# Optimization experiments

Hardware: AMD Instinct MI355X
Metric: run time of the kernel (lower is better)

Reference implementation:

```python
import jax, jax.numpy as jnp
import numpy as np

DIM = 2048
N_HEAD = 16
HEAD_DIM = DIM // N_HEAD


def setup_inputs() -> dict:
    key = jax.random.key(0)
    ks = jax.random.split(key, 7)
    B, N = 2, 2048
    s = 1.0 / np.sqrt(DIM)
    return {
        "x": jax.random.normal(ks[0], (B, N, DIM), dtype=jnp.float32),
        "Wq": jax.random.normal(ks[1], (DIM, DIM), dtype=jnp.float32) * s,
        "bq": jnp.zeros((DIM,), dtype=jnp.float32),
        "Wkv": jax.random.normal(ks[2], (DIM, 2 * HEAD_DIM), dtype=jnp.float32) * s,
        "bkv": jnp.zeros((2 * HEAD_DIM,), dtype=jnp.float32),
        "Wo": jax.random.normal(ks[3], (DIM, DIM), dtype=jnp.float32) * s,
        "bo": jnp.zeros((DIM,), dtype=jnp.float32),
    }


def reference(x, Wq, bq, Wkv, bkv, Wo, bo):
    B, N, D = x.shape
    # Q projection -> (B, H, N, hd)
    q = (x @ Wq + bq).reshape(B, N, N_HEAD, HEAD_DIM).transpose(0, 2, 1, 3)
    # shared single-head K/V (kv = x, self-attention path)
    kvp = x @ Wkv + bkv  # (B, M, 2*hd)
    k, v = kvp[..., :HEAD_DIM], kvp[..., HEAD_DIM:]  # (B, M, hd) each
    scale = 1.0 / np.sqrt(HEAD_DIM).astype(np.float32)
    # broadcast shared K over heads without materializing expanded K/V
    scores = jnp.einsum("bhnd,bmd->bhnm", q, k) * scale  # (B, H, N, M)
    attn = jax.nn.softmax(scores, axis=-1)
    out = jnp.einsum("bhnm,bmd->bhnd", attn, v)  # (B, H, N, hd)
    out = out.transpose(0, 2, 1, 3).reshape(B, N, D)
    return out @ Wo + bo
```

## Files before the change

kernel.cpp:

```cpp
#include <hip/hip_runtime.h>
#include <math.h>

using bf16x8 = __attribute__((ext_vector_type(8))) short;
using f32x4  = __attribute__((ext_vector_type(4))) float;
using f32x16 = __attribute__((ext_vector_type(16))) float;
using u16x4  = __attribute__((ext_vector_type(4))) unsigned short;
using u32x4  = __attribute__((ext_vector_type(4))) unsigned int;

#define DIMSZ 2048
#define NSEQ  2048
#define BATCH 2
#define NHEAD 16
#define HD    128

__device__ __forceinline__ unsigned short f2bf(float x) {
    unsigned int u = __builtin_bit_cast(unsigned int, x);
    unsigned int r = (u + 0x7FFFu + ((u >> 16) & 1u)) >> 16;
    return (unsigned short)r;
}

__device__ __forceinline__ unsigned int cvtpk_bf16(float lo, float hi) {
    unsigned int r;
    asm("v_cvt_pk_bf16_f32 %0, %1, %2" : "=v"(r) : "v"(lo), "v"(hi));
    return r;
}

__device__ __forceinline__ void gload_lds16(const unsigned short* g, unsigned short* l) {
    __builtin_amdgcn_global_load_lds(
        (const __attribute__((address_space(1))) unsigned int*)g,
        (__attribute__((address_space(3))) unsigned int*)l, 16, 0, 0);
}

#define NCAST 8192
__global__ void k_prep(const float* __restrict__ x, unsigned short* __restrict__ xb,
                       const float* __restrict__ Wq, const float* __restrict__ Wkv,
                       const float* __restrict__ Wo, unsigned short* __restrict__ wqkvt,
                       unsigned short* __restrict__ wot, float sc) {
    __shared__ float t[32][33];
    const int tid = threadIdx.x;
    if ((int)blockIdx.x < NCAST) {
        int i = blockIdx.x * 256 + tid;
        f32x4 v = *(const f32x4*)(x + (size_t)i * 4);
        u16x4 o;
#pragma unroll
        for (int j = 0; j < 4; j++) o[j] = f2bf(v[j]);
        *(u16x4*)(xb + (size_t)i * 4) = o;
        return;
    }
    const int tb = blockIdx.x - NCAST;
    const int ct = tb % 136;
    const int k0 = (tb / 136) * 32;
    const float* src;
    unsigned short* dst;
    float scale;
    int N, n0;
    if (ct < 64)      { src = Wq;  dst = wqkvt;                       scale = sc;   N = 2048; n0 = ct * 32; }
    else if (ct < 72) { src = Wkv; dst = wqkvt + (size_t)2048 * 2048; scale = 1.0f; N = 256;  n0 = (ct - 64) * 32; }
    else              { src = Wo;  dst = wot;                         scale = 1.0f; N = 2048; n0 = (ct - 72) * 32; }
    const int tx = tid & 31, ty = tid >> 5;
#pragma unroll
    for (int i = 0; i < 32; i += 8) t[ty + i][tx] = src[(size_t)(k0 + ty + i) * N + n0 + tx];
    __syncthreads();
#pragma unroll
    for (int i = 0; i < 32; i += 8)
        dst[(size_t)(n0 + ty + i) * 2048 + k0 + tx] = f2bf(t[tx][ty + i] * scale);
}

__device__ __forceinline__ void xcd_tile(int nbx, int& bx, int& by) {
    int wg = ((int)blockIdx.x & 7) * ((int)gridDim.x >> 3) + ((int)blockIdx.x >> 3);
    bx = wg % nbx;
    by = wg / nbx;
}

__global__ __launch_bounds__(256, 2)
void k_gemm_qkv(const unsigned short* __restrict__ A, const unsigned short* __restrict__ Bt,
                const float* __restrict__ bq, float bscale, const float* __restrict__ bkv,
                unsigned short* __restrict__ qout, unsigned short* __restrict__ kvout,
                unsigned short* __restrict__ vtout, int M, int K, int nbx) {
    __shared__ unsigned short As[2][128 * 32];
    __shared__ unsigned short Bs[2][128 * 32];
    const int tid = threadIdx.x;
    const int wid = tid >> 6;
    const int lane = tid & 63;
    const int g = lane >> 4, cc = lane & 15;
    const int wr = wid >> 1, wc = wid & 1;
    int bx, by;
    xcd_tile(nbx, bx, by);
    const size_t m0 = (size_t)by * 128;
    const size_t n0 = (size_t)bx * 128;

    f32x4 acc[4][4] = {};

    const int srow = wid * 32 + (lane >> 2);
    const int sch = lane & 3;
    const unsigned short* gA = A + (m0 + srow) * (size_t)K + sch * 8;
    const unsigned short* gB = Bt + (n0 + srow) * (size_t)K + sch * 8;
    const int lo = wid * 32 * 32;

    auto STAGE = [&](int buf, int k0) {
        gload_lds16(gA + k0, &As[buf][lo]);
        gload_lds16(gA + 16 * (size_t)K + k0, &As[buf][lo + 16 * 32]);
        gload_lds16(gB + k0, &Bs[buf][lo]);
        gload_lds16(gB + 16 * (size_t)K + k0, &Bs[buf][lo + 16 * 32]);
    };

    STAGE(0, 0);
    __syncthreads();
    int cur = 0;
    for (int k0 = 0; k0 < K; k0 += 32) {
        if (k0 + 32 < K) STAGE(cur ^ 1, k0 + 32);
        bf16x8 af[4], bfr[4];
#pragma unroll
        for (int mi = 0; mi < 4; mi++) af[mi] = *(const bf16x8*)(&As[cur][(wr * 64 + mi * 16 + cc) * 32 + g * 8]);
#pragma unroll
        for (int ni = 0; ni < 4; ni++) bfr[ni] = *(const bf16x8*)(&Bs[cur][(wc * 64 + ni * 16 + cc) * 32 + g * 8]);
#pragma unroll
        for (int mi = 0; mi < 4; mi++)
#pragma unroll
            for (int ni = 0; ni < 4; ni++)
                acc[mi][ni] = __builtin_amdgcn_mfma_f32_16x16x32_bf16(af[mi], bfr[ni], acc[mi][ni], 0, 0, 0);
        __syncthreads();
        cur ^= 1;
    }

    if (n0 < 2048) {
        const int col0 = (int)n0 + wc * 64 + cc;
        float bia[4];
#pragma unroll
        for (int ni = 0; ni < 4; ni++) bia[ni] = bq[col0 + ni * 16] * bscale;
#pragma unroll
        for (int mi = 0; mi < 4; mi++) {
            size_t row = m0 + wr * 64 + mi * 16 + g * 4;
#pragma unroll
            for (int ni = 0; ni < 4; ni++)
#pragma unroll
                for (int r = 0; r < 4; r++)
                    qout[(row + r) * 2048 + col0 + ni * 16] = f2bf(acc[mi][ni][r] + bia[ni]);
        }
    } else if (n0 < 2176) {
        const int col0 = (int)n0 - 2048 + wc * 64 + cc;
        float bia[4];
#pragma unroll
        for (int ni = 0; ni < 4; ni++) bia[ni] = bkv[col0 + ni * 16];
#pragma unroll
        for (int mi = 0; mi < 4; mi++) {
            size_t row = m0 + wr * 64 + mi * 16 + g * 4;
#pragma unroll
            for (int ni = 0; ni < 4; ni++)
#pragma unroll
                for (int r = 0; r < 4; r++)
                    kvout[(row + r) * 256 + col0 + ni * 16] = f2bf(acc[mi][ni][r] + bia[ni]);
        }
    } else {
        const int col0 = (int)n0 - 2048 + wc * 64 + cc;
        float bia[4];
#pragma unroll
        for (int ni = 0; ni < 4; ni++) bia[ni] = bkv[col0 + ni * 16];
#pragma unroll
        for (int mi = 0; mi < 4; mi++) {
            size_t row = m0 + wr * 64 + mi * 16 + g * 4;
            const int b = (int)(row >> 11);
            const int n = (int)(row & 2047);
#pragma unroll
            for (int ni = 0; ni < 4; ni++) {
                const int d = col0 + ni * 16 - 128;
                u16x4 o;
#pragma unroll
                for (int r = 0; r < 4; r++) o[r] = f2bf(acc[mi][ni][r] + bia[ni]);
                *(u16x4*)(vtout + ((size_t)(b * HD + d)) * NSEQ + n) = o;
            }
        }
    }
}

__global__ __launch_bounds__(256, 2)
void k_gemm_bt_f32(const unsigned short* __restrict__ A, const unsigned short* __restrict__ Bt,
                   const float* __restrict__ bias, float* __restrict__ Cout,
                   int M, int N, int K, int nbx) {
    __shared__ unsigned short As[2][128 * 32];
    __shared__ unsigned short Bs[2][128 * 32];
    const int tid = threadIdx.x;
    const int wid = tid >> 6;
    const int lane = tid & 63;
    const int g = lane >> 4, cc = lane & 15;
    const int wr = wid >> 1, wc = wid & 1;
    int bx, by;
    xcd_tile(nbx, bx, by);
    const size_t m0 = (size_t)by * 128;
    const size_t n0 = (size_t)bx * 128;

    f32x4 acc[4][4] = {};

    const int srow = wid * 32 + (lane >> 2);
    const int sch = lane & 3;
    const unsigned short* gA = A + (m0 + srow) * (size_t)K + sch * 8;
    const unsigned short* gB = Bt + (n0 + srow) * (size_t)K + sch * 8;
    const int lo = wid * 32 * 32;

    auto STAGE = [&](int buf, int k0) {
        gload_lds16(gA + k0, &As[buf][lo]);
        gload_lds16(gA + 16 * (size_t)K + k0, &As[buf][lo + 16 * 32]);
        gload_lds16(gB + k0, &Bs[buf][lo]);
        gload_lds16(gB + 16 * (size_t)K + k0, &Bs[buf][lo + 16 * 32]);
    };

    STAGE(0, 0);
    __syncthreads();
    int cur = 0;
    for (int k0 = 0; k0 < K; k0 += 32) {
        if (k0 + 32 < K) STAGE(cur ^ 1, k0 + 32);
        bf16x8 af[4], bfr[4];
#pragma unroll
        for (int mi = 0; mi < 4; mi++) af[mi] = *(const bf16x8*)(&As[cur][(wr * 64 + mi * 16 + cc) * 32 + g * 8]);
#pragma unroll
        for (int ni = 0; ni < 4; ni++) bfr[ni] = *(const bf16x8*)(&Bs[cur][(wc * 64 + ni * 16 + cc) * 32 + g * 8]);
#pragma unroll
        for (int mi = 0; mi < 4; mi++)
#pragma unroll
            for (int ni = 0; ni < 4; ni++)
                acc[mi][ni] = __builtin_amdgcn_mfma_f32_16x16x32_bf16(af[mi], bfr[ni], acc[mi][ni], 0, 0, 0);
        __syncthreads();
        cur ^= 1;
    }

    const int col0 = (int)n0 + wc * 64 + cc;
    float bia[4];
#pragma unroll
    for (int ni = 0; ni < 4; ni++) bia[ni] = bias[col0 + ni * 16];
#pragma unroll
    for (int mi = 0; mi < 4; mi++) {
        size_t row = m0 + wr * 64 + mi * 16 + g * 4;
#pragma unroll
        for (int ni = 0; ni < 4; ni++)
#pragma unroll
            for (int r = 0; r < 4; r++)
                Cout[(row + r) * N + col0 + ni * 16] = acc[mi][ni][r] + bia[ni];
    }
}

__global__ __launch_bounds__(256, 2)
void k_attn(const unsigned short* __restrict__ q, const unsigned short* __restrict__ kvp,
            const unsigned short* __restrict__ vt, unsigned short* __restrict__ out) {
    __shared__ unsigned char Kb[2][16384];
    __shared__ unsigned char Vb[2][16384];

    const int b = blockIdx.z, h = blockIdx.y, qt = blockIdx.x;
    const int tid = threadIdx.x, w = tid >> 6, lane = tid & 63;
    const int q32 = lane & 31, hi = lane >> 5;

    const int qrow = qt * 128 + w * 32 + q32;
    const unsigned short* qp = q + (size_t)(b * NSEQ + qrow) * DIMSZ + h * HD + hi * 8;
    bf16x8 qf[8];
#pragma unroll
    for (int dc = 0; dc < 8; dc++) qf[dc] = *(const bf16x8*)(qp + dc * 16);

    const char* kvpc = (const char*)kvp;
    const char* vtc  = (const char*)vt;
    size_t srcK[4], srcV[4];
#pragma unroll
    for (int c = 0; c < 4; c++) {
        unsigned int o = (tid + c * 256) * 16;
        unsigned int krow = o >> 8, kcol = o & 255;
        srcK[c] = (size_t)(b * NSEQ + krow) * 512 + (kcol ^ (((krow >> 1) & 15) << 4));
        unsigned int vrow = o >> 7, vcol = o & 127;
        srcV[c] = (size_t)(b * HD + vrow) * 4096 + (vcol ^ (((vrow >> 2) & 7) << 4));
    }

    auto STAGE = [&](int buf, int t) {
        size_t kb_ = (size_t)t * 32768;
        size_t vb_ = (size_t)t * 128;
#pragma unroll
        for (int c = 0; c < 4; c++) {
            gload_lds16((const unsigned short*)(kvpc + srcK[c] + kb_),
                        (unsigned short*)(Kb[buf] + (w * 64 + c * 256) * 16));
            gload_lds16((const unsigned short*)(vtc + srcV[c] + vb_),
                        (unsigned short*)(Vb[buf] + (w * 64 + c * 256) * 16));
        }
    };

    f32x16 o0 = {}, o1 = {}, o2 = {}, o3 = {};
    float l_run = 0.0f;
    const unsigned int swK = ((q32 >> 1) & 15) << 4;
    const unsigned int swV = ((q32 >> 2) & 7) << 4;

#define PROC_KT(S, KTB)                                                               \
    {                                                                                 \
        float pz[16];                                                                 \
        _Pragma("unroll") for (int r = 0; r < 16; r++) {                              \
            pz[r] = __builtin_amdgcn_exp2f(S[r]);                                     \
            l_run += pz[r];                                                           \
        }                                                                             \
        _Pragma("unroll") for (int kc = 0; kc < 2; kc++) {                            \
            unsigned int own01 = cvtpk_bf16(pz[kc * 8 + 0], pz[kc * 8 + 1]);          \
            unsigned int own23 = cvtpk_bf16(pz[kc * 8 + 2], pz[kc * 8 + 3]);          \
            unsigned int own45 = cvtpk_bf16(pz[kc * 8 + 4], pz[kc * 8 + 5]);          \
            unsigned int own67 = cvtpk_bf16(pz[kc * 8 + 6], pz[kc * 8 + 7]);          \
            unsigned int send_a = hi ? own01 : own45;                                 \
            unsigned int send_b = hi ? own23 : own67;                                 \
            unsigned int got_a = (unsigned int)__shfl_xor((int)send_a, 32, 64);       \
            unsigned int got_b = (unsigned int)__shfl_xor((int)send_b, 32, 64);       \
            u32x4 awv;                                                                \
            awv[0] = hi ? got_a : own01;                                              \
            awv[1] = hi ? got_b : own23;                                              \
            awv[2] = hi ? own45 : got_a;                                              \
            awv[3] = hi ? own67 : got_b;                                              \
            bf16x8 pa = __builtin_bit_cast(bf16x8, awv);                              \
            const unsigned int kbo = (KTB) + kc * 32 + hi * 16;                       \
            bf16x8 vf0 = *(const bf16x8*)(Vc + (q32 + 0) * 128 + (kbo ^ swV));        \
            bf16x8 vf1 = *(const bf16x8*)(Vc + (q32 + 32) * 128 + (kbo ^ swV));       \
            bf16x8 vf2 = *(const bf16x8*)(Vc + (q32 + 64) * 128 + (kbo ^ swV));       \
            bf16x8 vf3 = *(const bf16x8*)(Vc + (q32 + 96) * 128 + (kbo ^ swV));       \
            __builtin_amdgcn_s_setprio(1);                                            \
            o0 = __builtin_amdgcn_mfma_f32_32x32x16_bf16(pa, vf0, o0, 0, 0, 0);       \
            o1 = __builtin_amdgcn_mfma_f32_32x32x16_bf16(pa, vf1, o1, 0, 0, 0);       \
            o2 = __builtin_amdgcn_mfma_f32_32x32x16_bf16(pa, vf2, o2, 0, 0, 0);       \
            o3 = __builtin_amdgcn_mfma_f32_32x32x16_bf16(pa, vf3, o3, 0, 0, 0);       \
            __builtin_amdgcn_s_setprio(0);                                            \
        }                                                                             \
    }

    STAGE(0, 0);
    __syncthreads();

    for (int t = 0; t < NSEQ / 64; t++) {
        const int cur = t & 1;
        if (t < NSEQ / 64 - 1) STAGE(cur ^ 1, t + 1);

        const unsigned char* Kc = Kb[cur];
        const unsigned char* Vc = Vb[cur];

        f32x16 s0 = {}, s1 = {};
#pragma unroll
        for (int dc = 0; dc < 8; dc++) {
            const unsigned int db = dc * 32 + hi * 16;
            bf16x8 kf0 = *(const bf16x8*)(Kc + q32 * 256 + (db ^ swK));
            bf16x8 kf1 = *(const bf16x8*)(Kc + (q32 + 32) * 256 + (db ^ swK));
            __builtin_amdgcn_s_setprio(1);
            s0 = __builtin_amdgcn_mfma_f32_32x32x16_bf16(kf0, qf[dc], s0, 0, 0, 0);
            s1 = __builtin_amdgcn_mfma_f32_32x32x16_bf16(kf1, qf[dc], s1, 0, 0, 0);
            __builtin_amdgcn_s_setprio(0);
        }

        PROC_KT(s0, 0)
        PROC_KT(s1, 64)

        __syncthreads();
    }
#undef PROC_KT

    l_run += __shfl_xor(l_run, 32, 64);
    float* Lp = (float*)(Kb[0] + w * 128);
    if (hi == 0) Lp[q32] = l_run;

    float rinv[16];
#pragma unroll
    for (int r = 0; r < 16; r++) {
        int qloc = (r & 3) + 8 * (r >> 2) + 4 * hi;
        rinv[r] = 1.0f / Lp[qloc];
    }

    unsigned short* op = out + (size_t)(b * NSEQ + qt * 128 + w * 32) * DIMSZ + h * HD + q32;
#pragma unroll
    for (int r = 0; r < 16; r++) {
        int qloc = (r & 3) + 8 * (r >> 2) + 4 * hi;
        op[(size_t)qloc * DIMSZ + 0]  = f2bf(o0[r] * rinv[r]);
        op[(size_t)qloc * DIMSZ + 32] = f2bf(o1[r] * rinv[r]);
        op[(size_t)qloc * DIMSZ + 64] = f2bf(o2[r] * rinv[r]);
        op[(size_t)qloc * DIMSZ + 96] = f2bf(o3[r] * rinv[r]);
    }
}

extern "C" void kernel_launch(void* const* d_in, const int* in_sizes, int n_in,
                              void* d_out, int out_size, void* d_ws, size_t ws_size,
                              hipStream_t stream) {
    const float* x   = (const float*)d_in[0];
    const float* Wq  = (const float*)d_in[1];
    const float* bq  = (const float*)d_in[2];
    const float* Wkv = (const float*)d_in[3];
    const float* bkv = (const float*)d_in[4];
    const float* Wo  = (const float*)d_in[5];
    const float* bo  = (const float*)d_in[6];

    char* w = (char*)d_ws;
    unsigned short* xb    = (unsigned short*)(w);
    unsigned short* wqkvt = (unsigned short*)(w + 16777216);
    unsigned short* wot   = (unsigned short*)(w + 26214400);
    unsigned short* qb    = (unsigned short*)(w + 34603008);
    unsigned short* kvpb  = (unsigned short*)(w + 51380224);
    unsigned short* vtb   = (unsigned short*)(w + 53477376);
    unsigned short* aob   = xb;

    const float sc = 0.08838834764831845f * 1.4426950408889634f;

    k_prep<<<dim3(NCAST + 136 * 64), dim3(256), 0, stream>>>(x, xb, Wq, Wkv, Wo, wqkvt, wot, sc);

    k_gemm_qkv<<<dim3((2304 / 128) * (BATCH * NSEQ / 128)), dim3(256), 0, stream>>>(
        xb, wqkvt, bq, sc, bkv, qb, kvpb, vtb, BATCH * NSEQ, DIMSZ, 2304 / 128);
    k_attn<<<dim3(NSEQ / 128, NHEAD, BATCH), dim3(256), 0, stream>>>(qb, kvpb, vtb, aob);
    k_gemm_bt_f32<<<dim3((DIMSZ / 128) * (BATCH * NSEQ / 128)), dim3(256), 0, stream>>>(
        aob, wot, bo, (float*)d_out, BATCH * NSEQ, DIMSZ, DIMSZ, DIMSZ / 128);
}
```

Baseline: 200.2 us.

## Deepen output-projection GEMM K-tile to 64 with XOR-swizzled LDS layout

The f32-output GEMM (output projection) now stages 64-wide K slices per iteration instead of 32, halving the number of barriers and loop iterations. LDS rows are 128 bytes and the 16-byte granules are XOR-swizzled by row index, both when loading from global memory and when reading fragments, to avoid LDS bank conflicts. This doubles LDS use per block (64 KB total with double buffering), which may limit occupancy to the requested two blocks per CU.

```diff
diff --git a/kernel.cpp b/kernel.cpp
--- a/kernel.cpp
+++ b/kernel.cpp
@@ -177,8 +177,8 @@
 void k_gemm_bt_f32(const unsigned short* __restrict__ A, const unsigned short* __restrict__ Bt,
                    const float* __restrict__ bias, float* __restrict__ Cout,
                    int M, int N, int K, int nbx) {
-    __shared__ unsigned short As[2][128 * 32];
-    __shared__ unsigned short Bs[2][128 * 32];
+    __shared__ unsigned short As[2][128 * 64];
+    __shared__ unsigned short Bs[2][128 * 64];
     const int tid = threadIdx.x;
     const int wid = tid >> 6;
     const int lane = tid & 63;
@@ -191,34 +191,45 @@
 
     f32x4 acc[4][4] = {};
 
-    const int srow = wid * 32 + (lane >> 2);
-    const int sch = lane & 3;
-    const unsigned short* gA = A + (m0 + srow) * (size_t)K + sch * 8;
-    const unsigned short* gB = Bt + (n0 + srow) * (size_t)K + sch * 8;
-    const int lo = wid * 32 * 32;
+    const int srow = wid * 32 + (lane >> 3);
+    const int sgran = (lane & 7) ^ (lane >> 3);
+    const unsigned short* gA = A + (m0 + srow) * (size_t)K + sgran * 8;
+    const unsigned short* gB = Bt + (n0 + srow) * (size_t)K + sgran * 8;
 
     auto STAGE = [&](int buf, int k0) {
-        gload_lds16(gA + k0, &As[buf][lo]);
-        gload_lds16(gA + 16 * (size_t)K + k0, &As[buf][lo + 16 * 32]);
-        gload_lds16(gB + k0, &Bs[buf][lo]);
-        gload_lds16(gB + 16 * (size_t)K + k0, &Bs[buf][lo + 16 * 32]);
+#pragma unroll
+        for (int c = 0; c < 4; c++) {
+            gload_lds16(gA + (size_t)(c * 8) * K + k0, &As[buf][(wid * 32 + c * 8) * 64]);
+            gload_lds16(gB + (size_t)(c * 8) * K + k0, &Bs[buf][(wid * 32 + c * 8) * 64]);
+        }
     };
 
     STAGE(0, 0);
     __syncthreads();
     int cur = 0;
-    for (int k0 = 0; k0 < K; k0 += 32) {
-        if (k0 + 32 < K) STAGE(cur ^ 1, k0 + 32);
-        bf16x8 af[4], bfr[4];
-#pragma unroll
-        for (int mi = 0; mi < 4; mi++) af[mi] = *(const bf16x8*)(&As[cur][(wr * 64 + mi * 16 + cc) * 32 + g * 8]);
-#pragma unroll
-        for (int ni = 0; ni < 4; ni++) bfr[ni] = *(const bf16x8*)(&Bs[cur][(wc * 64 + ni * 16 + cc) * 32 + g * 8]);
-#pragma unroll
-        for (int mi = 0; mi < 4; mi++)
-#pragma unroll
-            for (int ni = 0; ni < 4; ni++)
-                acc[mi][ni] = __builtin_amdgcn_mfma_f32_16x16x32_bf16(af[mi], bfr[ni], acc[mi][ni], 0, 0, 0);
+    for (int k0 = 0; k0 < K; k0 += 64) {
+        if (k0 + 64 < K) STAGE(cur ^ 1, k0 + 64);
+#pragma unroll
+        for (int kk = 0; kk < 2; kk++) {
+            bf16x8 af[4], bfr[4];
+#pragma unroll
+            for (int mi = 0; mi < 4; mi++) {
+                const int row = wr * 64 + mi * 16 + cc;
+                af[mi] = *(const bf16x8*)((const unsigned char*)&As[cur][0] +
+                                          row * 128 + (((kk * 4 + g) ^ (row & 7)) * 16));
+            }
+#pragma unroll
+            for (int ni = 0; ni < 4; ni++) {
+                const int row = wc * 64 + ni * 16 + cc;
+                bfr[ni] = *(const bf16x8*)((const unsigned char*)&Bs[cur][0] +
+                                           row * 128 + (((kk * 4 + g) ^ (row & 7)) * 16));
+            }
+#pragma unroll
+            for (int mi = 0; mi < 4; mi++)
+#pragma unroll
+                for (int ni = 0; ni < 4; ni++)
+                    acc[mi][ni] = __builtin_amdgcn_mfma_f32_16x16x32_bf16(af[mi], bfr[ni], acc[mi][ni], 0, 0, 0);
+        }
         __syncthreads();
         cur ^= 1;
     }
```

Result: faster. 191.2 us (median of 2 runs) (-4.5%).
